# Kernel optimization log

Measured on AMD Instinct MI355X. Metric: run time of the kernel, lower is better.

Reference implementation:

```python
import math
import jax, jax.numpy as jnp
import numpy as np

HEAD_SIZE = 64
DEPTH = 0

def lambda_init_fn(depth):
    depth = depth + 1
    return 0.8 - 0.6 * math.exp(-0.3 * depth)

def setup_inputs() -> dict:
    key = jax.random.key(0)
    ks = jax.random.split(key, 9)
    B, T, C = 4, 4096, 1024
    H2 = 2 * HEAD_SIZE  # 128
    return {
        "x":  jax.random.normal(ks[0], (B, T, C), dtype=jnp.float32),
        "Wq": jax.random.normal(ks[1], (C, H2), dtype=jnp.float32) * (C ** -0.5),
        "Wk": jax.random.normal(ks[2], (C, H2), dtype=jnp.float32) * (C ** -0.5),
        "Wv": jax.random.normal(ks[3], (C, H2), dtype=jnp.float32) * (C ** -0.5),
        "lambda_q1": jax.random.normal(ks[4], (HEAD_SIZE,), dtype=jnp.float32) * 0.1,
        "lambda_q2": jax.random.normal(ks[5], (HEAD_SIZE,), dtype=jnp.float32) * 0.1,
        "lambda_k1": jax.random.normal(ks[6], (HEAD_SIZE,), dtype=jnp.float32) * 0.1,
        "lambda_k2": jax.random.normal(ks[7], (HEAD_SIZE,), dtype=jnp.float32) * 0.1,
    }

def reference(x, Wq, Wk, Wv, lambda_q1, lambda_q2, lambda_k1, lambda_k2):
    B, T, C = x.shape
    q = x @ Wq  # (B,T,2*hs)
    k = x @ Wk
    v = x @ Wv  # (B,T,2*hs)
    q1, q2 = jnp.split(q, 2, axis=-1)
    k1, k2 = jnp.split(k, 2, axis=-1)
    scale = 1.0 / math.sqrt(HEAD_SIZE)
    w1 = jnp.einsum('btd,bsd->bts', q1, k1) * scale  # (B,T,T)
    w2 = jnp.einsum('btd,bsd->bts', q2, k2) * scale
    causal = jnp.tril(jnp.ones((T, T), dtype=bool))
    neg_inf = jnp.float32(-jnp.inf)
    w1 = jnp.where(causal, w1, neg_inf)
    w2 = jnp.where(causal, w2, neg_inf)
    lam1 = jnp.exp(jnp.sum(lambda_q1 * lambda_k1))
    lam2 = jnp.exp(jnp.sum(lambda_q2 * lambda_k2))
    lam = lam1 - lam2 + lambda_init_fn(DEPTH)
    weights = jax.nn.softmax(w1, axis=-1) - lam * jax.nn.softmax(w2, axis=-1)
    out = jnp.einsum('bts,bsd->btd', weights, v)  # (B,T,2*hs)
    return out
```

## Files before the change

kernel.cpp:

```cpp
#include <hip/hip_runtime.h>
#include <hip/hip_bf16.h>

typedef __bf16 bf16x8 __attribute__((ext_vector_type(8)));
typedef float f32x4 __attribute__((ext_vector_type(4)));

#define LOG2E 1.4426950408889634f
#define LAMBDA_INIT 0.3555090675909693f
#define CEXP 0.18033688011112042f
#define MOFF 11.541560327111708f

#define K_OFF   ((size_t)16384 * 128)
#define VT_OFF  ((size_t)2 * 16384 * 128)
#define PART_OFF_BYTES ((size_t)12582912)
#define WT_OFF_BYTES   ((size_t)46661632)
#define REC_FLOATS 4160

__device__ __forceinline__ unsigned short f2bf(float f) {
    __hip_bfloat16 h = __float2bfloat16(f);
    unsigned short u;
    __builtin_memcpy(&u, &h, 2);
    return u;
}
__device__ __forceinline__ float bf2f(unsigned short u) {
    unsigned int x = ((unsigned int)u) << 16;
    float f;
    __builtin_memcpy(&f, &x, 4);
    return f;
}
__device__ __forceinline__ unsigned int cvt_pk_bf16(float a, float b) {
    unsigned int r;
    asm volatile("v_cvt_pk_bf16_f32 %0, %1, %2" : "=v"(r) : "v"(a), "v"(b));
    return r;
}

__global__ __launch_bounds__(256) void prep_wt(
    const float* __restrict__ Wq, const float* __restrict__ Wk,
    const float* __restrict__ Wv, unsigned short* __restrict__ WT) {
    const int kt = blockIdx.x, nt = blockIdx.y, mat = blockIdx.z;
    const float* W = (mat == 0) ? Wq : (mat == 1) ? Wk : Wv;
    unsigned short* O = WT + (size_t)mat * 128 * 1024;
    __shared__ float tb[64][65];
    const int r = threadIdx.x >> 2, c4 = (threadIdx.x & 3) * 16;
    for (int j = 0; j < 4; ++j) {
        float4 v = *(const float4*)&W[(size_t)(kt * 64 + r) * 128 + nt * 64 + c4 + j * 4];
        tb[r][c4 + j * 4 + 0] = v.x;
        tb[r][c4 + j * 4 + 1] = v.y;
        tb[r][c4 + j * 4 + 2] = v.z;
        tb[r][c4 + j * 4 + 3] = v.w;
    }
    __syncthreads();
    unsigned short tmp[16];
    for (int j = 0; j < 16; ++j) tmp[j] = f2bf(tb[c4 + j][r]);
    *(uint4*)&O[(size_t)(nt * 64 + r) * 1024 + kt * 64 + c4] = *(uint4*)&tmp[0];
    *(uint4*)&O[(size_t)(nt * 64 + r) * 1024 + kt * 64 + c4 + 8] = *(uint4*)&tmp[8];
}

__global__ __launch_bounds__(256) void qkv_gemm(
    const float* __restrict__ x, const unsigned short* __restrict__ WT,
    unsigned short* __restrict__ qkv) {
    const int tid = threadIdx.x;
    const int l = tid & 63, wid = tid >> 6;
    const int g = l >> 4, i16 = l & 15;
    const int row0 = blockIdx.x * 128;
    const int mat = blockIdx.y;
    const unsigned short* Wt = WT + (size_t)mat * 128 * 1024;

    __shared__ unsigned short smem[2][128][72];
    auto xs = smem[0];
    auto wt = smem[1];

    f32x4 acc[2][8];
    const f32x4 z4 = {0.f, 0.f, 0.f, 0.f};
    for (int a = 0; a < 2; ++a)
        for (int b = 0; b < 8; ++b) acc[a][b] = z4;

    for (int k0 = 0; k0 < 1024; k0 += 64) {
        __syncthreads();
        {
            const int c = (tid & 15) * 4;
            const int rbase = tid >> 4;
            #pragma unroll
            for (int it = 0; it < 8; ++it) {
                int r = rbase + it * 16;
                const float4 v = *(const float4*)&x[(size_t)(row0 + r) * 1024 + k0 + c];
                ushort4 pk = make_ushort4(f2bf(v.x), f2bf(v.y), f2bf(v.z), f2bf(v.w));
                *(ushort4*)&xs[r][c] = pk;
            }
        }
        {
            #pragma unroll
            for (int it = 0; it < 4; ++it) {
                int lin = it * 256 + tid;
                int n = lin >> 3, k8 = (lin & 7) * 8;
                *(uint4*)&wt[n][k8] = *(const uint4*)&Wt[(size_t)n * 1024 + k0 + k8];
            }
        }
        __syncthreads();

        bf16x8 af[2][2];
        for (int rb = 0; rb < 2; ++rb)
            for (int c = 0; c < 2; ++c)
                af[rb][c] = *(const bf16x8*)&xs[wid * 32 + rb * 16 + i16][c * 32 + 8 * g];
        for (int nb = 0; nb < 8; ++nb) {
            bf16x8 b0 = *(const bf16x8*)&wt[nb * 16 + i16][8 * g];
            bf16x8 b1 = *(const bf16x8*)&wt[nb * 16 + i16][32 + 8 * g];
            for (int rb = 0; rb < 2; ++rb) {
                acc[rb][nb] = __builtin_amdgcn_mfma_f32_16x16x32_bf16(af[rb][0], b0, acc[rb][nb], 0, 0, 0);
                acc[rb][nb] = __builtin_amdgcn_mfma_f32_16x16x32_bf16(af[rb][1], b1, acc[rb][nb], 0, 0, 0);
            }
        }
    }

    __syncthreads();
    unsigned short(*ts)[136] = (unsigned short(*)[136]) & smem[0][0][0];
    for (int rb = 0; rb < 2; ++rb)
        for (int nb = 0; nb < 8; ++nb)
            for (int r = 0; r < 4; ++r)
                ts[wid * 32 + rb * 16 + g * 4 + r][nb * 16 + i16] = f2bf(acc[rb][nb][r]);
    __syncthreads();

    const int bq = row0 >> 12;
    const int s0b = (row0 & 4095) >> 6;
    if (mat == 0) {
        unsigned short* outp = qkv + (size_t)row0 * 128;
        #pragma unroll
        for (int it = 0; it < 8; ++it) {
            int tr = it * 16 + (tid >> 4), dv0 = (tid & 15) * 8;
            *(uint4*)&outp[tr * 128 + dv0] = *(const uint4*)&ts[tr][dv0];
        }
    } else if (mat == 1) {
        unsigned short* kimg = qkv + K_OFF;
        #pragma unroll
        for (int it = 0; it < 8; ++it) {
            int lin = it * 256 + tid;
            int tile = lin >> 10;
            int branch_ = (lin >> 9) & 1;
            int region = (lin >> 6) & 7;
            int slot = lin & 63;
            int row = tile * 64 + (region >> 1) * 16 + (slot & 15);
            int d = branch_ * 64 + (region & 1) * 32 + (slot >> 4) * 8;
            uint4 vv = *(const uint4*)&ts[row][d];
            size_t off = ((size_t)((bq * 64 + s0b + tile) * 2 + branch_) * 4096) + (region * 64 + slot) * 8;
            *(uint4*)&kimg[off] = vv;
        }
    } else {
        unsigned short* vimg = qkv + VT_OFF;
        #pragma unroll
        for (int it = 0; it < 8; ++it) {
            int lin = it * 256 + tid;
            int tile = lin >> 10;
            int rem = lin & 1023;
            int region = rem >> 6;
            int slot = rem & 63;
            int dv = (region >> 1) * 16 + (slot & 15);
            int kv0 = (region & 1) * 32 + (slot >> 4) * 8;
            unsigned short tmp[8];
            #pragma unroll
            for (int e = 0; e < 8; ++e) tmp[e] = ts[tile * 64 + kv0 + e][dv];
            size_t off = ((size_t)(bq * 64 + s0b + tile) * 8192) + (region * 64 + slot) * 8;
            *(uint4*)&vimg[off] = *(uint4*)tmp;
        }
    }
}

__global__ __launch_bounds__(256) void diff_attn_pair(
    const unsigned short* __restrict__ q, const unsigned short* __restrict__ kimg,
    const unsigned short* __restrict__ vimg,
    float* __restrict__ part) {
    const int bx = blockIdx.x, b = blockIdx.y;
    const int c = blockIdx.z >> 1, branch = blockIdx.z & 1;

    const int tid = threadIdx.x;
    const int l = tid & 63, w = tid >> 6;
    const int gq = l >> 4, i16 = l & 15;
    const float NEGINF = -__builtin_inff();

    __shared__ unsigned short ksf[4096];
    __shared__ unsigned short vtf[8192];
    __shared__ unsigned short psf[4096];

    const int tid8 = tid * 8;
    int pdst[4];
    #pragma unroll
    for (int cb = 0; cb < 4; ++cb)
        pdst[cb] = ((w * 2 + (cb >> 1)) * 64 + ((cb & 1) * 2 + (gq >> 1)) * 16 + i16) * 8 + (gq & 1) * 4;
    const int prd0 = ((w * 2 + 0) * 64 + l) * 8;
    const int prd1 = ((w * 2 + 1) * 64 + l) * 8;

    const size_t bbase = (size_t)b * 4096;
    const unsigned short* kimg_b = kimg + (size_t)b * 524288;
    const unsigned short* vimg_b = vimg + (size_t)b * 524288;
    const f32x4 z4 = {0.f, 0.f, 0.f, 0.f};
    uint4 kr0, kr1, vr0, vr1, vr2, vr3;

#define KV_LOAD(s_) do {                                                            \
        const unsigned short* kp = &kimg_b[((size_t)(s_) * 2 + branch) * 4096];     \
        kr0 = *(const uint4*)&kp[tid8];                                             \
        kr1 = *(const uint4*)&kp[tid8 + 2048];                                      \
        const unsigned short* vp = &vimg_b[(size_t)(s_) * 8192];                    \
        vr0 = *(const uint4*)&vp[tid8];                                             \
        vr1 = *(const uint4*)&vp[tid8 + 2048];                                      \
        vr2 = *(const uint4*)&vp[tid8 + 4096];                                      \
        vr3 = *(const uint4*)&vp[tid8 + 6144];                                      \
    } while (0)

#define KV_STORE() do {                                                             \
        *(uint4*)&ksf[tid8] = kr0;                                                  \
        *(uint4*)&ksf[tid8 + 2048] = kr1;                                           \
        *(uint4*)&vtf[tid8] = vr0;                                                  \
        *(uint4*)&vtf[tid8 + 2048] = vr1;                                           \
        *(uint4*)&vtf[tid8 + 4096] = vr2;                                           \
        *(uint4*)&vtf[tid8 + 6144] = vr3;                                           \
    } while (0)

    #pragma unroll 1
    for (int seg = 0; seg < 2; ++seg) {
        const int t = seg ? (63 - bx) : bx;
        const int n = t + 1;
        const int s0 = (c * n) >> 2, smax = ((c + 1) * n) >> 2;

        float* rec = part + ((((size_t)b * 64 + t) * 4 + c) * 2 + branch) * REC_FLOATS;
        if (s0 >= smax) {
            unsigned int* pz = (unsigned int*)rec;
            for (int i = tid; i < REC_FLOATS; i += 256) pz[i] = 0u;
            continue;
        }

        bf16x8 qf[2];
        for (int cc = 0; cc < 2; ++cc)
            qf[cc] = *(const bf16x8*)&q[(bbase + t * 64 + w * 16 + i16) * 128 + branch * 64 + cc * 32 + 8 * gq];

        float lsum = 0.f;
        f32x4 acc_o[8];
        for (int nb = 0; nb < 8; ++nb) acc_o[nb] = z4;

        KV_LOAD(s0);
        #pragma unroll 1
        for (int s = s0; s < smax; ++s) {
            __syncthreads();
            KV_STORE();
            if (s + 1 < smax) KV_LOAD(s + 1);
            __syncthreads();

            f32x4 sc[4];
            for (int cb = 0; cb < 4; ++cb) sc[cb] = z4;
            __builtin_amdgcn_s_setprio(1);
            #pragma unroll
            for (int cb = 0; cb < 4; ++cb)
                for (int cc = 0; cc < 2; ++cc) {
                    bf16x8 kf = *(const bf16x8*)&ksf[((cb * 2 + cc) * 64 + l) * 8];
                    sc[cb] = __builtin_amdgcn_mfma_f32_16x16x32_bf16(kf, qf[cc], sc[cb], 0, 0, 0);
                }
            __builtin_amdgcn_s_setprio(0);
            if (s == t) {
                int ql = w * 16 + i16;
                for (int cb = 0; cb < 4; ++cb)
                    for (int r = 0; r < 4; ++r)
                        if (cb * 16 + gq * 4 + r > ql) sc[cb][r] = NEGINF;
            }
            #pragma unroll
            for (int cb = 0; cb < 4; ++cb)
                for (int r = 0; r < 4; ++r) {
                    float pv = exp2f(fmaf(sc[cb][r], CEXP, -MOFF));
                    sc[cb][r] = pv;
                    lsum += pv;
                }
            #pragma unroll
            for (int cb = 0; cb < 4; ++cb) {
                uint2 pw;
                pw.x = cvt_pk_bf16(sc[cb][0], sc[cb][1]);
                pw.y = cvt_pk_bf16(sc[cb][2], sc[cb][3]);
                *(uint2*)&psf[pdst[cb]] = pw;
            }
            asm volatile("s_waitcnt lgkmcnt(0)" ::: "memory");
            bf16x8 pa0 = *(const bf16x8*)&psf[prd0];
            bf16x8 pa1 = *(const bf16x8*)&psf[prd1];
            __builtin_amdgcn_s_setprio(1);
            #pragma unroll
            for (int nb = 0; nb < 8; ++nb) {
                bf16x8 vb0 = *(const bf16x8*)&vtf[((nb * 2 + 0) * 64 + l) * 8];
                acc_o[nb] = __builtin_amdgcn_mfma_f32_16x16x32_bf16(pa0, vb0, acc_o[nb], 0, 0, 0);
                bf16x8 vb1 = *(const bf16x8*)&vtf[((nb * 2 + 1) * 64 + l) * 8];
                acc_o[nb] = __builtin_amdgcn_mfma_f32_16x16x32_bf16(pa1, vb1, acc_o[nb], 0, 0, 0);
            }
            __builtin_amdgcn_s_setprio(0);
        }

        lsum += __shfl_xor(lsum, 16);
        lsum += __shfl_xor(lsum, 32);
        unsigned short* Orec = (unsigned short*)(rec + 64);
        if (gq == 0) rec[w * 16 + i16] = lsum;
        for (int nb = 0; nb < 8; ++nb)
            for (int r = 0; r < 4; ++r) {
                int row = w * 16 + gq * 4 + r;
                Orec[row * 128 + nb * 16 + i16] = f2bf(acc_o[nb][r]);
            }
    }
#undef KV_LOAD
#undef KV_STORE
}

__global__ __launch_bounds__(256) void diff_combine(
    const float* __restrict__ part,
    const float* __restrict__ lq1, const float* __restrict__ lq2,
    const float* __restrict__ lk1, const float* __restrict__ lk2,
    float* __restrict__ out) {
    const int t = blockIdx.x, b = blockIdx.y;
    const int tid = threadIdx.x;
    __shared__ float sl[2][64];
    __shared__ float s_lam;

    const float* recbase = part + (((size_t)b * 64 + t) * 4) * 2 * REC_FLOATS;

    if (tid < 64) {
        float s1 = lq1[tid] * lk1[tid];
        float s2 = lq2[tid] * lk2[tid];
        for (int off = 32; off > 0; off >>= 1) {
            s1 += __shfl_xor(s1, off);
            s2 += __shfl_xor(s2, off);
        }
        if (tid == 0) s_lam = expf(s1) - expf(s2) + LAMBDA_INIT;
    }
    if (tid < 128) {
        int r = tid & 63, br = tid >> 6;
        float acc = 0.f;
        for (int c = 0; c < 4; ++c) acc += recbase[(c * 2 + br) * REC_FLOATS + r];
        sl[br][r] = acc;
    }
    __syncthreads();
    const float lam = s_lam;

    float* op = out + ((size_t)b * 4096 + (size_t)t * 64) * 128;
    for (int grp = 0; grp < 4; ++grp) {
        int gid = grp * 256 + tid;
        int e = gid * 8;
        int row = e >> 7;
        float o1[8] = {0, 0, 0, 0, 0, 0, 0, 0}, o2[8] = {0, 0, 0, 0, 0, 0, 0, 0};
        #pragma unroll
        for (int c = 0; c < 4; ++c) {
            const unsigned short* O0 = (const unsigned short*)(recbase + (c * 2 + 0) * REC_FLOATS + 64);
            const unsigned short* O1 = (const unsigned short*)(recbase + (c * 2 + 1) * REC_FLOATS + 64);
            uint4 u0 = *(const uint4*)&O0[e];
            uint4 u1 = *(const uint4*)&O1[e];
            const unsigned short* e0 = (const unsigned short*)&u0;
            const unsigned short* e1 = (const unsigned short*)&u1;
            #pragma unroll
            for (int j = 0; j < 8; ++j) {
                o1[j] += bf2f(e0[j]);
                o2[j] += bf2f(e1[j]);
            }
        }
        float l1inv = 1.0f / sl[0][row], l2inv = 1.0f / sl[1][row];
        float res[8];
        #pragma unroll
        for (int j = 0; j < 8; ++j) res[j] = o1[j] * l1inv - lam * o2[j] * l2inv;
        *(float4*)&op[e] = *(float4*)&res[0];
        *(float4*)&op[e + 4] = *(float4*)&res[4];
    }
}

extern "C" void kernel_launch(void* const* d_in, const int* in_sizes, int n_in,
                              void* d_out, int out_size, void* d_ws, size_t ws_size,
                              hipStream_t stream) {
    const float* x   = (const float*)d_in[0];
    const float* Wq  = (const float*)d_in[1];
    const float* Wk  = (const float*)d_in[2];
    const float* Wv  = (const float*)d_in[3];
    const float* lq1 = (const float*)d_in[4];
    const float* lq2 = (const float*)d_in[5];
    const float* lk1 = (const float*)d_in[6];
    const float* lk2 = (const float*)d_in[7];
    float* out = (float*)d_out;
    unsigned short* qkv = (unsigned short*)d_ws;
    float* part = (float*)((char*)d_ws + PART_OFF_BYTES);
    unsigned short* WT = (unsigned short*)((char*)d_ws + WT_OFF_BYTES);

    prep_wt<<<dim3(16, 2, 3), 256, 0, stream>>>(Wq, Wk, Wv, WT);
    qkv_gemm<<<dim3(128, 3), 256, 0, stream>>>(x, WT, qkv);

    const unsigned short* qb = qkv;
    const unsigned short* kb = qkv + K_OFF;
    const unsigned short* vtb = qkv + VT_OFF;
    diff_attn_pair<<<dim3(32, 4, 8), 256, 0, stream>>>(qb, kb, vtb, part);
    diff_combine<<<dim3(64, 4), 256, 0, stream>>>(part, lq1, lq2, lk1, lk2, out);
}
```

Before: 102.8 us.

## Process adjacent query tiles together to share K/V loads in attention kernel

Each block now handles two adjacent query tiles (t_e, t_o) over the same key range instead of two mirrored tiles in sequence, so each K tile in shared memory and each V fragment is used by both query tiles. V is loaded straight into registers, split by output column across waves, which removes the V shared-memory staging. The P@V product is regrouped so each wave owns output columns rather than query rows, and occupancy is hinted with launch bounds of 3 blocks per SU. The cost is more registers, an extra barrier per iteration, and different load balancing across blocks. The host launch grid likely has to change to match the new tile pairing.

```diff
diff --git a/kernel.cpp b/kernel.cpp
--- a/kernel.cpp
+++ b/kernel.cpp
@@ -163,12 +163,15 @@
     }
 }
 
-__global__ __launch_bounds__(256) void diff_attn_pair(
+__global__ __launch_bounds__(256, 3) void diff_attn_pair(
     const unsigned short* __restrict__ q, const unsigned short* __restrict__ kimg,
     const unsigned short* __restrict__ vimg,
     float* __restrict__ part) {
     const int bx = blockIdx.x, b = blockIdx.y;
     const int c = blockIdx.z >> 1, branch = blockIdx.z & 1;
+    const int t_o = 63 - 2 * bx, t_e = t_o - 1;
+    const int n = t_o + 1;
+    const int s_lo = (c * n) >> 2, smax = ((c + 1) * n) >> 2;
 
     const int tid = threadIdx.x;
     const int l = tid & 63, w = tid >> 6;
@@ -176,72 +179,76 @@
     const float NEGINF = -__builtin_inff();
 
     __shared__ unsigned short ksf[4096];
-    __shared__ unsigned short vtf[8192];
-    __shared__ unsigned short psf[4096];
-
+    __shared__ unsigned short psf[8192];
+
+    float* recA = part + ((((size_t)b * 64 + t_e) * 4 + c) * 2 + branch) * REC_FLOATS;
+    float* recB = part + ((((size_t)b * 64 + t_o) * 4 + c) * 2 + branch) * REC_FLOATS;
+
+    if (s_lo >= smax) {
+        unsigned int* pa_ = (unsigned int*)recA;
+        unsigned int* pb_ = (unsigned int*)recB;
+        for (int i = tid; i < REC_FLOATS; i += 256) { pa_[i] = 0u; pb_[i] = 0u; }
+        return;
+    }
+    const bool emptyA = (s_lo > t_e);
+    if (emptyA) {
+        unsigned int* pa_ = (unsigned int*)recA;
+        for (int i = tid; i < REC_FLOATS; i += 256) pa_[i] = 0u;
+    }
+
+    const size_t bbase = (size_t)b * 4096;
+    const unsigned short* kimg_b = kimg + (size_t)b * 524288;
+    const unsigned short* vimg_b = vimg + (size_t)b * 524288;
     const int tid8 = tid * 8;
+    const int l8 = l * 8;
+    const f32x4 z4 = {0.f, 0.f, 0.f, 0.f};
+
+    bf16x8 qfA[2], qfB[2];
+    #pragma unroll
+    for (int cc = 0; cc < 2; ++cc) {
+        qfA[cc] = *(const bf16x8*)&q[(bbase + t_e * 64 + w * 16 + i16) * 128 + branch * 64 + cc * 32 + 8 * gq];
+        qfB[cc] = *(const bf16x8*)&q[(bbase + t_o * 64 + w * 16 + i16) * 128 + branch * 64 + cc * 32 + 8 * gq];
+    }
+
+    float lsumA = 0.f, lsumB = 0.f;
+    f32x4 acc[2][4][2];
+    for (int qs = 0; qs < 2; ++qs)
+        for (int qg = 0; qg < 4; ++qg)
+            for (int j = 0; j < 2; ++j) acc[qs][qg][j] = z4;
+
     int pdst[4];
     #pragma unroll
     for (int cb = 0; cb < 4; ++cb)
         pdst[cb] = ((w * 2 + (cb >> 1)) * 64 + ((cb & 1) * 2 + (gq >> 1)) * 16 + i16) * 8 + (gq & 1) * 4;
-    const int prd0 = ((w * 2 + 0) * 64 + l) * 8;
-    const int prd1 = ((w * 2 + 1) * 64 + l) * 8;
-
-    const size_t bbase = (size_t)b * 4096;
-    const unsigned short* kimg_b = kimg + (size_t)b * 524288;
-    const unsigned short* vimg_b = vimg + (size_t)b * 524288;
-    const f32x4 z4 = {0.f, 0.f, 0.f, 0.f};
-    uint4 kr0, kr1, vr0, vr1, vr2, vr3;
-
-#define KV_LOAD(s_) do {                                                            \
+
+    uint4 kr0, kr1;
+    bf16x8 vb00, vb01, vb10, vb11;
+
+#define K_ISSUE(s_) do {                                                            \
         const unsigned short* kp = &kimg_b[((size_t)(s_) * 2 + branch) * 4096];     \
         kr0 = *(const uint4*)&kp[tid8];                                             \
         kr1 = *(const uint4*)&kp[tid8 + 2048];                                      \
-        const unsigned short* vp = &vimg_b[(size_t)(s_) * 8192];                    \
-        vr0 = *(const uint4*)&vp[tid8];                                             \
-        vr1 = *(const uint4*)&vp[tid8 + 2048];                                      \
-        vr2 = *(const uint4*)&vp[tid8 + 4096];                                      \
-        vr3 = *(const uint4*)&vp[tid8 + 6144];                                      \
     } while (0)
-
-#define KV_STORE() do {                                                             \
-        *(uint4*)&ksf[tid8] = kr0;                                                  \
-        *(uint4*)&ksf[tid8 + 2048] = kr1;                                           \
-        *(uint4*)&vtf[tid8] = vr0;                                                  \
-        *(uint4*)&vtf[tid8 + 2048] = vr1;                                           \
-        *(uint4*)&vtf[tid8 + 4096] = vr2;                                           \
-        *(uint4*)&vtf[tid8 + 6144] = vr3;                                           \
+#define V_ISSUE(s_) do {                                                            \
+        const unsigned short* vp = &vimg_b[(size_t)(s_) * 8192 + w * 2048];         \
+        vb00 = *(const bf16x8*)&vp[l8];                                             \
+        vb01 = *(const bf16x8*)&vp[512 + l8];                                       \
+        vb10 = *(const bf16x8*)&vp[1024 + l8];                                      \
+        vb11 = *(const bf16x8*)&vp[1536 + l8];                                      \
     } while (0)
 
+    K_ISSUE(s_lo);
+    V_ISSUE(s_lo);
     #pragma unroll 1
-    for (int seg = 0; seg < 2; ++seg) {
-        const int t = seg ? (63 - bx) : bx;
-        const int n = t + 1;
-        const int s0 = (c * n) >> 2, smax = ((c + 1) * n) >> 2;
-
-        float* rec = part + ((((size_t)b * 64 + t) * 4 + c) * 2 + branch) * REC_FLOATS;
-        if (s0 >= smax) {
-            unsigned int* pz = (unsigned int*)rec;
-            for (int i = tid; i < REC_FLOATS; i += 256) pz[i] = 0u;
-            continue;
-        }
-
-        bf16x8 qf[2];
-        for (int cc = 0; cc < 2; ++cc)
-            qf[cc] = *(const bf16x8*)&q[(bbase + t * 64 + w * 16 + i16) * 128 + branch * 64 + cc * 32 + 8 * gq];
-
-        float lsum = 0.f;
-        f32x4 acc_o[8];
-        for (int nb = 0; nb < 8; ++nb) acc_o[nb] = z4;
-
-        KV_LOAD(s0);
-        #pragma unroll 1
-        for (int s = s0; s < smax; ++s) {
-            __syncthreads();
-            KV_STORE();
-            if (s + 1 < smax) KV_LOAD(s + 1);
-            __syncthreads();
-
+    for (int s = s_lo; s < smax; ++s) {
+        __syncthreads();
+        *(uint4*)&ksf[tid8] = kr0;
+        *(uint4*)&ksf[tid8 + 2048] = kr1;
+        if (s + 1 < smax) K_ISSUE(s + 1);
+        __syncthreads();
+        const bool aAct = (s != t_o);
+
+        if (aAct) {
             f32x4 sc[4];
             for (int cb = 0; cb < 4; ++cb) sc[cb] = z4;
             __builtin_amdgcn_s_setprio(1);
@@ -249,55 +256,107 @@
             for (int cb = 0; cb < 4; ++cb)
                 for (int cc = 0; cc < 2; ++cc) {
                     bf16x8 kf = *(const bf16x8*)&ksf[((cb * 2 + cc) * 64 + l) * 8];
-                    sc[cb] = __builtin_amdgcn_mfma_f32_16x16x32_bf16(kf, qf[cc], sc[cb], 0, 0, 0);
+                    sc[cb] = __builtin_amdgcn_mfma_f32_16x16x32_bf16(kf, qfA[cc], sc[cb], 0, 0, 0);
                 }
             __builtin_amdgcn_s_setprio(0);
-            if (s == t) {
+            if (s == t_e) {
                 int ql = w * 16 + i16;
                 for (int cb = 0; cb < 4; ++cb)
                     for (int r = 0; r < 4; ++r)
                         if (cb * 16 + gq * 4 + r > ql) sc[cb][r] = NEGINF;
             }
             #pragma unroll
+            for (int cb = 0; cb < 4; ++cb) {
+                float p0 = exp2f(fmaf(sc[cb][0], CEXP, -MOFF));
+                float p1 = exp2f(fmaf(sc[cb][1], CEXP, -MOFF));
+                float p2 = exp2f(fmaf(sc[cb][2], CEXP, -MOFF));
+                float p3 = exp2f(fmaf(sc[cb][3], CEXP, -MOFF));
+                lsumA += (p0 + p1) + (p2 + p3);
+                uint2 pw;
+                pw.x = cvt_pk_bf16(p0, p1);
+                pw.y = cvt_pk_bf16(p2, p3);
+                *(uint2*)&psf[pdst[cb]] = pw;
+            }
+        }
+        {
+            f32x4 sc[4];
+            for (int cb = 0; cb < 4; ++cb) sc[cb] = z4;
+            __builtin_amdgcn_s_setprio(1);
+            #pragma unroll
             for (int cb = 0; cb < 4; ++cb)
-                for (int r = 0; r < 4; ++r) {
-                    float pv = exp2f(fmaf(sc[cb][r], CEXP, -MOFF));
-                    sc[cb][r] = pv;
-                    lsum += pv;
+                for (int cc = 0; cc < 2; ++cc) {
+                    bf16x8 kf = *(const bf16x8*)&ksf[((cb * 2 + cc) * 64 + l) * 8];
+                    sc[cb] = __builtin_amdgcn_mfma_f32_16x16x32_bf16(kf, qfB[cc], sc[cb], 0, 0, 0);
                 }
+            __builtin_amdgcn_s_setprio(0);
+            if (s == t_o) {
+                int ql = w * 16 + i16;
+                for (int cb = 0; cb < 4; ++cb)
+                    for (int r = 0; r < 4; ++r)
+                        if (cb * 16 + gq * 4 + r > ql) sc[cb][r] = NEGINF;
+            }
             #pragma unroll
             for (int cb = 0; cb < 4; ++cb) {
+                float p0 = exp2f(fmaf(sc[cb][0], CEXP, -MOFF));
+                float p1 = exp2f(fmaf(sc[cb][1], CEXP, -MOFF));
+                float p2 = exp2f(fmaf(sc[cb][2], CEXP, -MOFF));
+                float p3 = exp2f(fmaf(sc[cb][3], CEXP, -MOFF));
+                lsumB += (p0 + p1) + (p2 + p3);
                 uint2 pw;
-                pw.x = cvt_pk_bf16(sc[cb][0], sc[cb][1]);
-                pw.y = cvt_pk_bf16(sc[cb][2], sc[cb][3]);
-                *(uint2*)&psf[pdst[cb]] = pw;
-            }
-            asm volatile("s_waitcnt lgkmcnt(0)" ::: "memory");
-            bf16x8 pa0 = *(const bf16x8*)&psf[prd0];
-            bf16x8 pa1 = *(const bf16x8*)&psf[prd1];
-            __builtin_amdgcn_s_setprio(1);
-            #pragma unroll
-            for (int nb = 0; nb < 8; ++nb) {
-                bf16x8 vb0 = *(const bf16x8*)&vtf[((nb * 2 + 0) * 64 + l) * 8];
-                acc_o[nb] = __builtin_amdgcn_mfma_f32_16x16x32_bf16(pa0, vb0, acc_o[nb], 0, 0, 0);
-                bf16x8 vb1 = *(const bf16x8*)&vtf[((nb * 2 + 1) * 64 + l) * 8];
-                acc_o[nb] = __builtin_amdgcn_mfma_f32_16x16x32_bf16(pa1, vb1, acc_o[nb], 0, 0, 0);
-            }
-            __builtin_amdgcn_s_setprio(0);
-        }
-
-        lsum += __shfl_xor(lsum, 16);
-        lsum += __shfl_xor(lsum, 32);
-        unsigned short* Orec = (unsigned short*)(rec + 64);
-        if (gq == 0) rec[w * 16 + i16] = lsum;
-        for (int nb = 0; nb < 8; ++nb)
-            for (int r = 0; r < 4; ++r) {
-                int row = w * 16 + gq * 4 + r;
-                Orec[row * 128 + nb * 16 + i16] = f2bf(acc_o[nb][r]);
-            }
-    }
-#undef KV_LOAD
-#undef KV_STORE
+                pw.x = cvt_pk_bf16(p0, p1);
+                pw.y = cvt_pk_bf16(p2, p3);
+                *(uint2*)&psf[4096 + pdst[cb]] = pw;
+            }
+        }
+        __syncthreads();
+
+        __builtin_amdgcn_s_setprio(1);
+        if (aAct) {
+            #pragma unroll
+            for (int qg = 0; qg < 4; ++qg) {
+                bf16x8 pa0 = *(const bf16x8*)&psf[(qg * 2 + 0) * 512 + l8];
+                bf16x8 pa1 = *(const bf16x8*)&psf[(qg * 2 + 1) * 512 + l8];
+                acc[0][qg][0] = __builtin_amdgcn_mfma_f32_16x16x32_bf16(pa0, vb00, acc[0][qg][0], 0, 0, 0);
+                acc[0][qg][0] = __builtin_amdgcn_mfma_f32_16x16x32_bf16(pa1, vb01, acc[0][qg][0], 0, 0, 0);
+                acc[0][qg][1] = __builtin_amdgcn_mfma_f32_16x16x32_bf16(pa0, vb10, acc[0][qg][1], 0, 0, 0);
+                acc[0][qg][1] = __builtin_amdgcn_mfma_f32_16x16x32_bf16(pa1, vb11, acc[0][qg][1], 0, 0, 0);
+            }
+        }
+        #pragma unroll
+        for (int qg = 0; qg < 4; ++qg) {
+            bf16x8 pa0 = *(const bf16x8*)&psf[4096 + (qg * 2 + 0) * 512 + l8];
+            bf16x8 pa1 = *(const bf16x8*)&psf[4096 + (qg * 2 + 1) * 512 + l8];
+            acc[1][qg][0] = __builtin_amdgcn_mfma_f32_16x16x32_bf16(pa0, vb00, acc[1][qg][0], 0, 0, 0);
+            acc[1][qg][0] = __builtin_amdgcn_mfma_f32_16x16x32_bf16(pa1, vb01, acc[1][qg][0], 0, 0, 0);
+            acc[1][qg][1] = __builtin_amdgcn_mfma_f32_16x16x32_bf16(pa0, vb10, acc[1][qg][1], 0, 0, 0);
+            acc[1][qg][1] = __builtin_amdgcn_mfma_f32_16x16x32_bf16(pa1, vb11, acc[1][qg][1], 0, 0, 0);
+        }
+        __builtin_amdgcn_s_setprio(0);
+        if (s + 1 < smax) V_ISSUE(s + 1);
+    }
+#undef K_ISSUE
+#undef V_ISSUE
+
+    lsumA += __shfl_xor(lsumA, 16);
+    lsumA += __shfl_xor(lsumA, 32);
+    lsumB += __shfl_xor(lsumB, 16);
+    lsumB += __shfl_xor(lsumB, 32);
+    if (!emptyA) {
+        if (gq == 0) recA[w * 16 + i16] = lsumA;
+        unsigned short* OA = (unsigned short*)(recA + 64);
+        for (int qg = 0; qg < 4; ++qg)
+            for (int j = 0; j < 2; ++j)
+                for (int r = 0; r < 4; ++r)
+                    OA[(qg * 16 + gq * 4 + r) * 128 + (w * 2 + j) * 16 + i16] = f2bf(acc[0][qg][j][r]);
+    }
+    {
+        if (gq == 0) recB[w * 16 + i16] = lsumB;
+        unsigned short* OB = (unsigned short*)(recB + 64);
+        for (int qg = 0; qg < 4; ++qg)
+            for (int j = 0; j < 2; ++j)
+                for (int r = 0; r < 4; ++r)
+                    OB[(qg * 16 + gq * 4 + r) * 128 + (w * 2 + j) * 16 + i16] = f2bf(acc[1][qg][j][r]);
+    }
 }
 
 __global__ __launch_bounds__(256) void diff_combine(
```

New measurement: 112.7 us. 1.1x slower.
